# Optimization experiments

Hardware: AMD Instinct MI355X
Metric: run time of the kernel (lower is better)

The kernel has to match this reference:

```python
import jax, jax.numpy as jnp
import numpy as np

P, T, D = 2, 8192, 2048  # path_num (top-2), tokens per flow, feature dim

def setup_inputs() -> dict:
    key = jax.random.key(0)
    kd, k1, k2 = jax.random.split(key, 3)
    flows_data = jax.random.normal(kd, (P, T, D), dtype=jnp.float32)
    # Each flow's tags are a permutation of arange(T): union of tags covers
    # [0, T) exactly, so unique count == load == T (top-2 MoE combine).
    flows_tag = jnp.stack([
        jax.random.permutation(k1, T),
        jax.random.permutation(k2, T),
    ]).astype(jnp.int64)
    return {"flows_data": flows_data, "flows_tag": flows_tag, "load": T}

def reference(flows_data, flows_tag, load):
    # torch.cat(in_flows_data, dim=0) / torch.cat(in_flows_tag, dim=0)
    p, t, d = flows_data.shape
    data = flows_data.reshape(p * t, d)          # [P*T, D]
    tags = flows_tag.reshape(-1)                 # [P*T]
    # sparse=True path: torch.unique(sorted=True, return_inverse=True)
    # size=load is the static unique count (tags cover [0, load) by construction)
    _, inverse = jnp.unique(tags, return_inverse=True, size=load, fill_value=0)
    # zeros(load, D).scatter_(0, route_indices, data, reduce='add')
    out = jax.ops.segment_sum(data, inverse.reshape(-1), num_segments=load)  # [load, D]
    return out
```

## Files before the change

### kernel.cpp

```cpp
#include <hip/hip_runtime.h>


__global__ void build_inverse_kernel(const int* __restrict__ tags,
                                     int* __restrict__ inv,
                                     int T, int N) {
    int i = blockIdx.x * blockDim.x + threadIdx.x;
    if (i < N) {
        int p = i / T;
        int pos = i - p * T;
        int t = tags[i];
        inv[p * T + t] = pos;
    }
}

__global__ void gather_add_kernel(const float4* __restrict__ data,
                                  const int* __restrict__ inv,
                                  float4* __restrict__ out,
                                  int T, int D4) {
    int row = blockIdx.x;
    int i0 = inv[row];
    int i1 = inv[T + row];
    const float4* a = data + (size_t)i0 * D4;
    const float4* b = data + ((size_t)T + (size_t)i1) * D4;
    float4* o = out + (size_t)row * D4;
    for (int c = threadIdx.x; c < D4; c += blockDim.x) {
        float4 va = a[c];
        float4 vb = b[c];
        float4 v;
        v.x = va.x + vb.x;
        v.y = va.y + vb.y;
        v.z = va.z + vb.z;
        v.w = va.w + vb.w;
        o[c] = v;
    }
}

extern "C" void kernel_launch(void* const* d_in, const int* in_sizes, int n_in,
                              void* d_out, int out_size, void* d_ws, size_t ws_size,
                              hipStream_t stream) {
    const float* data = (const float*)d_in[0];
    const int* tags   = (const int*)d_in[1];

    const int N  = in_sizes[1];
    const int D  = in_sizes[0] / N;
    const int T  = out_size / D;
    const int D4 = D / 4;

    int* inv = (int*)d_ws;

    build_inverse_kernel<<<(N + 255) / 256, 256, 0, stream>>>(tags, inv, T, N);

    gather_add_kernel<<<T, 256, 0, stream>>>((const float4*)data, inv,
                                             (float4*)d_out, T, D4);
}
```

Before: 40.02 us.

## Fuse inverse build and gather-add into one cooperative kernel with nontemporal access

Merges the inverse-index scatter and the row gather-add into a single cooperative kernel. A grid-wide sync separates the two phases, removing one kernel launch and the gap between launches. The gather loop uses nontemporal loads and stores for the streaming data and is persistent over a fixed grid of 1024 blocks. The trade-off is the grid-sync cost and a cooperative launch that fails if 1024 blocks cannot all be resident at once.

```diff
diff --git a/kernel.cpp b/kernel.cpp
--- a/kernel.cpp
+++ b/kernel.cpp
@@ -1,55 +1,65 @@
 #include <hip/hip_runtime.h>
+#include <hip/hip_cooperative_groups.h>
+
+namespace cg = cooperative_groups;
 
 
-__global__ void build_inverse_kernel(const int* __restrict__ tags,
-                                     int* __restrict__ inv,
-                                     int T, int N) {
-    int i = blockIdx.x * blockDim.x + threadIdx.x;
-    if (i < N) {
-        int p = i / T;
+typedef float f32x4 __attribute__((ext_vector_type(4)));
+
+#define NBLOCKS  1024
+#define NTHREADS 256
+
+__global__ __launch_bounds__(NTHREADS, 4)
+void fused_router_kernel(const f32x4* __restrict__ data,
+                         const int*   __restrict__ tags,
+                         int*         __restrict__ inv,
+                         f32x4*       __restrict__ out,
+                         int T, int D4, int N) {
+    cg::grid_group grid = cg::this_grid();
+
+    int gtid = blockIdx.x * NTHREADS + threadIdx.x;
+    int gsz  = gridDim.x * NTHREADS;
+    for (int i = gtid; i < N; i += gsz) {
+        int p   = (i >= T) ? 1 : 0;
         int pos = i - p * T;
-        int t = tags[i];
-        inv[p * T + t] = pos;
+        inv[p * T + tags[i]] = pos;
     }
-}
 
-__global__ void gather_add_kernel(const float4* __restrict__ data,
-                                  const int* __restrict__ inv,
-                                  float4* __restrict__ out,
-                                  int T, int D4) {
-    int row = blockIdx.x;
-    int i0 = inv[row];
-    int i1 = inv[T + row];
-    const float4* a = data + (size_t)i0 * D4;
-    const float4* b = data + ((size_t)T + (size_t)i1) * D4;
-    float4* o = out + (size_t)row * D4;
-    for (int c = threadIdx.x; c < D4; c += blockDim.x) {
-        float4 va = a[c];
-        float4 vb = b[c];
-        float4 v;
-        v.x = va.x + vb.x;
-        v.y = va.y + vb.y;
-        v.z = va.z + vb.z;
-        v.w = va.w + vb.w;
-        o[c] = v;
+    __threadfence();
+    grid.sync();
+
+    for (int row = blockIdx.x; row < T; row += gridDim.x) {
+        int i0 = inv[row];
+        int i1 = inv[T + row];
+        const f32x4* a = data + (size_t)i0 * D4;
+        const f32x4* b = data + ((size_t)T + (size_t)i1) * D4;
+        f32x4* o = out + (size_t)row * D4;
+        for (int c = threadIdx.x; c < D4; c += NTHREADS) {
+            f32x4 va = __builtin_nontemporal_load(a + c);
+            f32x4 vb = __builtin_nontemporal_load(b + c);
+            __builtin_nontemporal_store(va + vb, o + c);
+        }
     }
 }
 
 extern "C" void kernel_launch(void* const* d_in, const int* in_sizes, int n_in,
                               void* d_out, int out_size, void* d_ws, size_t ws_size,
                               hipStream_t stream) {
-    const float* data = (const float*)d_in[0];
-    const int* tags   = (const int*)d_in[1];
+    const f32x4* data = (const f32x4*)d_in[0];
+    const int*   tags = (const int*)d_in[1];
 
     const int N  = in_sizes[1];
     const int D  = in_sizes[0] / N;
-    const int T  = out_size / D;
-    const int D4 = D / 4;
+    int T        = out_size / D;
+    int D4       = D / 4;
+    int Nmut     = N;
 
     int* inv = (int*)d_ws;
 
-    build_inverse_kernel<<<(N + 255) / 256, 256, 0, stream>>>(tags, inv, T, N);
-
-    gather_add_kernel<<<T, 256, 0, stream>>>((const float4*)data, inv,
-                                             (float4*)d_out, T, D4);
+    f32x4* out = (f32x4*)d_out;
+    void* args[] = {(void*)&data, (void*)&tags, (void*)&inv, (void*)&out,
+                    (void*)&T, (void*)&D4, (void*)&Nmut};
+    hipLaunchCooperativeKernel((void*)fused_router_kernel,
+                               dim3(NBLOCKS), dim3(NTHREADS),
+                               args, 0, stream);
 }
```

Result: slower. 153.0 us (+282.3%).
